# Performance work log

Measured on AMD Instinct MI355X. Metric: run time of the kernel, lower is better.

## Reference

```python
import jax, jax.numpy as jnp
import numpy as np

N_NODES = 100000
K = 50000  # ceil(ratio * N) with ratio = nodes_out / nodes_in = 0.5


def setup_inputs() -> dict:
    key = jax.random.key(0)
    k1, k2, k3 = jax.random.split(key, 3)
    x = jax.random.normal(k1, (N_NODES, 256), dtype=jnp.float32)
    edge_index = jax.random.randint(k2, (2, 3200000), 0, N_NODES, dtype=jnp.int64)
    weight = jax.random.normal(k3, (256,), dtype=jnp.float32)
    return {"x": x, "edge_index": edge_index, "weight": weight}


def reference(x, edge_index, weight):
    # --- PyG TopKPooling forward ---
    # score_i = tanh( <x_i, w> / ||w|| )
    score = jnp.tanh((x @ weight) / jnp.linalg.norm(weight))  # [N]
    # select top-k nodes by score
    top_scores, perm = jax.lax.top_k(score, K)  # [K], [K]
    # gather features and gate by score (multiplier)
    x_out = x[perm] * top_scores[:, None]  # [K, C]
    # --- filter_adj: keep edges whose endpoints both survive, remap ids ---
    mapping = jnp.full((x.shape[0],), -1, dtype=edge_index.dtype)
    mapping = mapping.at[perm].set(jnp.arange(K, dtype=edge_index.dtype))
    new_edges = mapping[edge_index]  # [2, E], -1 where endpoint dropped
    valid = (new_edges[0] >= 0) & (new_edges[1] >= 0)
    # fixed-shape output: invalid edges marked -1 (torch returns a compacted
    # variable-length tensor; we keep E fixed for jit-compatibility)
    edge_out = jnp.where(valid[None, :], new_edges, -1)
    return x_out, edge_out
```

## Files before the change

### kernel.cpp

```cpp
#include <hip/hip_runtime.h>
#include <math.h>

#define N_NODES 100000
#define N_FEAT  256
#define K_SEL   50000
#define N_EDGES 3200000
#define NBUCKET 65536

#define GATHER_BLOCKS (K_SEL / 4)
#define EDGE_BLOCKS   (N_EDGES / (4 * 256))

__device__ __forceinline__ unsigned long long descKey(double z) {
    unsigned long long u = (unsigned long long)__double_as_longlong(z);
    unsigned long long a = (u >> 63) ? ~u : (u | 0x8000000000000000ULL);
    return ~a;
}

__device__ __forceinline__ unsigned int bucketOfFloat(float zf) {
    unsigned int u = __float_as_uint(zf);
    unsigned int a = (u >> 31) ? ~u : (u | 0x80000000u);
    return (~a) >> 16;
}

__global__ void init_kernel(const float* __restrict__ w, double* __restrict__ norm,
                            int* __restrict__ hist) {
    __shared__ double sd[256];
    int t = blockIdx.x * blockDim.x + threadIdx.x;
    hist[t] = 0;
    if (blockIdx.x == 0) {
        int tt = threadIdx.x;
        double v = (double)w[tt];
        sd[tt] = v * v;
        __syncthreads();
        for (int off = 128; off > 0; off >>= 1) {
            if (tt < off) sd[tt] += sd[tt + off];
            __syncthreads();
        }
        if (tt == 0) norm[0] = sqrt(sd[0]);
    }
}

__global__ void score_kernel(const float* __restrict__ x, const float* __restrict__ w,
                             unsigned long long* __restrict__ key64,
                             float* __restrict__ dotf, int* __restrict__ hist) {
    int row  = (int)((blockIdx.x * blockDim.x + threadIdx.x) >> 6);
    int lane = threadIdx.x & 63;
    if (row >= N_NODES) return;
    const float4 xv = ((const float4*)(x + (size_t)row * N_FEAT))[lane];
    const float4 wv = ((const float4*)w)[lane];
    double acc = (double)xv.x * (double)wv.x + (double)xv.y * (double)wv.y +
                 (double)xv.z * (double)wv.z + (double)xv.w * (double)wv.w;
    for (int m = 32; m >= 1; m >>= 1) acc += __shfl_xor(acc, m, 64);
    if (lane == 0) {
        key64[row] = descKey(acc);
        float df = (float)acc;
        dotf[row] = df;
        atomicAdd(&hist[bucketOfFloat(df)], 1);
    }
}

__global__ void __launch_bounds__(1024) scan_kernel(const int4* __restrict__ hist4,
                                                    int* __restrict__ start) {
    __shared__ int sums[1024];
    int t = threadIdx.x;
    int4 v[16];
#pragma unroll
    for (int j = 0; j < 16; ++j) v[j] = hist4[t * 16 + j];
    int s = 0;
#pragma unroll
    for (int j = 0; j < 16; ++j) { s += v[j].x + v[j].y + v[j].z + v[j].w; }
    sums[t] = s;
    __syncthreads();
    for (int off = 1; off < 1024; off <<= 1) {
        int vv = (t >= off) ? sums[t - off] : 0;
        __syncthreads();
        sums[t] += vv;
        __syncthreads();
    }
    int run = (t == 0) ? 0 : sums[t - 1];
    int4* start4 = (int4*)start;
#pragma unroll
    for (int j = 0; j < 16; ++j) {
        int4 o;
        o.x = run; run += v[j].x;
        o.y = run; run += v[j].y;
        o.z = run; run += v[j].z;
        o.w = run; run += v[j].w;
        start4[t * 16 + j] = o;
    }
}

__global__ void scatter_kernel(const unsigned long long* __restrict__ key64,
                               const float* __restrict__ dotf,
                               int* __restrict__ start,
                               unsigned long long* __restrict__ slotKey,
                               int* __restrict__ slotIdx) {
    int i = blockIdx.x * blockDim.x + threadIdx.x;
    if (i >= N_NODES) return;
    int b = (int)bucketOfFloat(dotf[i]);
    int pos = atomicAdd(&start[b], 1);
    slotKey[pos] = key64[i];
    slotIdx[pos] = i;
}

__global__ void rank_kernel(const unsigned long long* __restrict__ slotKey,
                            const int* __restrict__ slotIdx,
                            const int* __restrict__ start, const int* __restrict__ hist,
                            const float* __restrict__ dotf,
                            int* __restrict__ mapping, int* __restrict__ perm,
                            float* __restrict__ selDot) {
    int s = blockIdx.x * blockDim.x + threadIdx.x;
    if (s >= N_NODES) return;
    unsigned long long myKey = slotKey[s];
    int i = slotIdx[s];
    float df = dotf[i];
    int b = (int)bucketOfFloat(df);
    int end = start[b];
    int cnt = hist[b];
    int st = end - cnt;
    int rank = 0;
    for (int t = st; t < end; ++t) {
        unsigned long long k = slotKey[t];
        if (k < myKey || (k == myKey && slotIdx[t] < i)) ++rank;
    }
    int p = st + rank;
    if (p < K_SEL) {
        mapping[i] = p;
        perm[p] = i;
        selDot[p] = df;
    } else {
        mapping[i] = -1;
    }
}

__global__ void out_kernel(const float* __restrict__ x, const int* __restrict__ perm,
                           const float* __restrict__ selDot,
                           const double* __restrict__ normp,
                           const int* __restrict__ ei, const int* __restrict__ mapping,
                           float* __restrict__ out) {
    if (blockIdx.x < GATHER_BLOCKS) {
        int tid = blockIdx.x * 256 + threadIdx.x;
        int r = tid >> 6;
        int c = (tid & 63) << 2;
        int src = perm[r];
        float sc = tanhf(selDot[r] / (float)normp[0]);
        float4 v = *(const float4*)(x + (size_t)src * N_FEAT + c);
        float4 o;
        o.x = v.x * sc; o.y = v.y * sc; o.z = v.z * sc; o.w = v.w * sc;
        *(float4*)(out + (size_t)r * N_FEAT + c) = o;
    } else {
        int tid = (blockIdx.x - GATHER_BLOCKS) * 256 + threadIdx.x;
        int e = tid << 2;
        int4 a = *(const int4*)(ei + e);
        int4 b = *(const int4*)(ei + N_EDGES + e);
        float* oeu = out + (size_t)K_SEL * N_FEAT;
        float* oev = oeu + N_EDGES;
        int m0 = mapping[a.x], m1 = mapping[a.y], m2 = mapping[a.z], m3 = mapping[a.w];
        int n0 = mapping[b.x], n1 = mapping[b.y], n2 = mapping[b.z], n3 = mapping[b.w];
        float4 ou, ov;
        bool v0 = (m0 >= 0) && (n0 >= 0);
        bool v1 = (m1 >= 0) && (n1 >= 0);
        bool v2 = (m2 >= 0) && (n2 >= 0);
        bool v3 = (m3 >= 0) && (n3 >= 0);
        ou.x = v0 ? (float)m0 : -1.0f; ov.x = v0 ? (float)n0 : -1.0f;
        ou.y = v1 ? (float)m1 : -1.0f; ov.y = v1 ? (float)n1 : -1.0f;
        ou.z = v2 ? (float)m2 : -1.0f; ov.z = v2 ? (float)n2 : -1.0f;
        ou.w = v3 ? (float)m3 : -1.0f; ov.w = v3 ? (float)n3 : -1.0f;
        *(float4*)(oeu + e) = ou;
        *(float4*)(oev + e) = ov;
    }
}

extern "C" void kernel_launch(void* const* d_in, const int* in_sizes, int n_in,
                              void* d_out, int out_size, void* d_ws, size_t ws_size,
                              hipStream_t stream) {
    const float* x  = (const float*)d_in[0];
    const int*   ei = (const int*)d_in[1];
    const float* w  = (const float*)d_in[2];
    float* out = (float*)d_out;

    char* p = (char*)d_ws;
    double* d_norm = (double*)p;                          p += 16;
    unsigned long long* key64   = (unsigned long long*)p; p += (size_t)N_NODES * 8;
    unsigned long long* slotKey = (unsigned long long*)p; p += (size_t)N_NODES * 8;
    float* dotf   = (float*)p;  p += (size_t)N_NODES * 4;
    int*   mapping= (int*)p;    p += (size_t)N_NODES * 4;
    int*   slotIdx= (int*)p;    p += (size_t)N_NODES * 4;
    int*   perm   = (int*)p;    p += (size_t)K_SEL * 4;
    float* selDot = (float*)p;  p += (size_t)K_SEL * 4;
    int*   hist   = (int*)p;    p += (size_t)NBUCKET * 4;
    int*   start  = (int*)p;    p += (size_t)NBUCKET * 4;

    init_kernel<<<NBUCKET / 256, 256, 0, stream>>>(w, d_norm, hist);

    int waves_blocks = (N_NODES * 64 + 255) / 256;
    score_kernel<<<waves_blocks, 256, 0, stream>>>(x, w, key64, dotf, hist);

    scan_kernel<<<1, 1024, 0, stream>>>((const int4*)hist, start);

    int node_blocks = (N_NODES + 255) / 256;
    scatter_kernel<<<node_blocks, 256, 0, stream>>>(key64, dotf, start, slotKey, slotIdx);

    rank_kernel<<<node_blocks, 256, 0, stream>>>(slotKey, slotIdx, start, hist, dotf,
                                                 mapping, perm, selDot);

    out_kernel<<<GATHER_BLOCKS + EDGE_BLOCKS, 256, 0, stream>>>(x, perm, selDot, d_norm,
                                                                ei, mapping, out);
}
```

Measured before the change: 319.6 us.

## Parallelize histogram scan, shrink mapping to 16-bit, replace init kernel with memset

Replaces the single-block 1024-thread histogram scan with a two-level scan: 256 blocks scan chunks, then one block scans the chunk sums and also computes the inverse weight norm. The init kernel becomes a hipMemsetAsync. The node mapping table is stored as 16-bit values with 0xFFFF as sentinel, halving the footprint of the table used by the random edge lookups. This adds one kernel launch and relies on K fitting in 16 bits.

```diff
diff --git a/kernel.cpp b/kernel.cpp
--- a/kernel.cpp
+++ b/kernel.cpp
@@ -6,6 +6,7 @@
 #define K_SEL   50000
 #define N_EDGES 3200000
 #define NBUCKET 65536
+#define NCHUNK  (NBUCKET / 256)
 
 #define GATHER_BLOCKS (K_SEL / 4)
 #define EDGE_BLOCKS   (N_EDGES / (4 * 256))
@@ -20,24 +21,6 @@
     unsigned int u = __float_as_uint(zf);
     unsigned int a = (u >> 31) ? ~u : (u | 0x80000000u);
     return (~a) >> 16;
-}
-
-__global__ void init_kernel(const float* __restrict__ w, double* __restrict__ norm,
-                            int* __restrict__ hist) {
-    __shared__ double sd[256];
-    int t = blockIdx.x * blockDim.x + threadIdx.x;
-    hist[t] = 0;
-    if (blockIdx.x == 0) {
-        int tt = threadIdx.x;
-        double v = (double)w[tt];
-        sd[tt] = v * v;
-        __syncthreads();
-        for (int off = 128; off > 0; off >>= 1) {
-            if (tt < off) sd[tt] += sd[tt + off];
-            __syncthreads();
-        }
-        if (tt == 0) norm[0] = sqrt(sd[0]);
-    }
 }
 
 __global__ void score_kernel(const float* __restrict__ x, const float* __restrict__ w,
@@ -59,63 +42,75 @@
     }
 }
 
-__global__ void __launch_bounds__(1024) scan_kernel(const int4* __restrict__ hist4,
-                                                    int* __restrict__ start) {
-    __shared__ int sums[1024];
+__global__ void scanA_kernel(const int* __restrict__ hist, int* __restrict__ partial,
+                             int* __restrict__ chunkSum) {
+    __shared__ int tmp[256];
     int t = threadIdx.x;
-    int4 v[16];
-#pragma unroll
-    for (int j = 0; j < 16; ++j) v[j] = hist4[t * 16 + j];
-    int s = 0;
-#pragma unroll
-    for (int j = 0; j < 16; ++j) { s += v[j].x + v[j].y + v[j].z + v[j].w; }
-    sums[t] = s;
+    int g = blockIdx.x * 256 + t;
+    int v = hist[g];
+    tmp[t] = v;
     __syncthreads();
-    for (int off = 1; off < 1024; off <<= 1) {
-        int vv = (t >= off) ? sums[t - off] : 0;
-        __syncthreads();
-        sums[t] += vv;
-        __syncthreads();
-    }
-    int run = (t == 0) ? 0 : sums[t - 1];
-    int4* start4 = (int4*)start;
-#pragma unroll
-    for (int j = 0; j < 16; ++j) {
-        int4 o;
-        o.x = run; run += v[j].x;
-        o.y = run; run += v[j].y;
-        o.z = run; run += v[j].z;
-        o.w = run; run += v[j].w;
-        start4[t * 16 + j] = o;
-    }
+    for (int off = 1; off < 256; off <<= 1) {
+        int u = (t >= off) ? tmp[t - off] : 0;
+        __syncthreads();
+        tmp[t] += u;
+        __syncthreads();
+    }
+    partial[g] = tmp[t] - v;
+    if (t == 255) chunkSum[blockIdx.x] = tmp[255];
+}
+
+__global__ void scanB_kernel(const int* __restrict__ chunkSum, int* __restrict__ offs,
+                             const float* __restrict__ w, float* __restrict__ invNorm) {
+    __shared__ int tmp[256];
+    __shared__ double sd[256];
+    int t = threadIdx.x;
+    int v = chunkSum[t];
+    tmp[t] = v;
+    double wv = (double)w[t];
+    sd[t] = wv * wv;
+    __syncthreads();
+    for (int off = 1; off < 256; off <<= 1) {
+        int u = (t >= off) ? tmp[t - off] : 0;
+        __syncthreads();
+        tmp[t] += u;
+        __syncthreads();
+    }
+    offs[t] = tmp[t] - v;
+    for (int off = 128; off > 0; off >>= 1) {
+        if (t < off) sd[t] += sd[t + off];
+        __syncthreads();
+    }
+    if (t == 0) invNorm[0] = (float)(1.0 / sqrt(sd[0]));
 }
 
 __global__ void scatter_kernel(const unsigned long long* __restrict__ key64,
                                const float* __restrict__ dotf,
-                               int* __restrict__ start,
+                               const int* __restrict__ offs, int* __restrict__ partial,
                                unsigned long long* __restrict__ slotKey,
                                int* __restrict__ slotIdx) {
     int i = blockIdx.x * blockDim.x + threadIdx.x;
     if (i >= N_NODES) return;
     int b = (int)bucketOfFloat(dotf[i]);
-    int pos = atomicAdd(&start[b], 1);
+    int pos = offs[b >> 8] + atomicAdd(&partial[b], 1);
     slotKey[pos] = key64[i];
     slotIdx[pos] = i;
 }
 
 __global__ void rank_kernel(const unsigned long long* __restrict__ slotKey,
                             const int* __restrict__ slotIdx,
-                            const int* __restrict__ start, const int* __restrict__ hist,
+                            const int* __restrict__ offs, const int* __restrict__ partial,
+                            const int* __restrict__ hist,
                             const float* __restrict__ dotf,
-                            int* __restrict__ mapping, int* __restrict__ perm,
-                            float* __restrict__ selDot) {
+                            unsigned short* __restrict__ mapping16,
+                            int* __restrict__ perm, float* __restrict__ selDot) {
     int s = blockIdx.x * blockDim.x + threadIdx.x;
     if (s >= N_NODES) return;
     unsigned long long myKey = slotKey[s];
     int i = slotIdx[s];
     float df = dotf[i];
     int b = (int)bucketOfFloat(df);
-    int end = start[b];
+    int end = offs[b >> 8] + partial[b];
     int cnt = hist[b];
     int st = end - cnt;
     int rank = 0;
@@ -125,25 +120,26 @@
     }
     int p = st + rank;
     if (p < K_SEL) {
-        mapping[i] = p;
+        mapping16[i] = (unsigned short)p;
         perm[p] = i;
         selDot[p] = df;
     } else {
-        mapping[i] = -1;
+        mapping16[i] = 0xFFFFu;
     }
 }
 
 __global__ void out_kernel(const float* __restrict__ x, const int* __restrict__ perm,
                            const float* __restrict__ selDot,
-                           const double* __restrict__ normp,
-                           const int* __restrict__ ei, const int* __restrict__ mapping,
+                           const float* __restrict__ invNormp,
+                           const int* __restrict__ ei,
+                           const unsigned short* __restrict__ mapping16,
                            float* __restrict__ out) {
     if (blockIdx.x < GATHER_BLOCKS) {
         int tid = blockIdx.x * 256 + threadIdx.x;
         int r = tid >> 6;
         int c = (tid & 63) << 2;
         int src = perm[r];
-        float sc = tanhf(selDot[r] / (float)normp[0]);
+        float sc = tanhf(selDot[r] * invNormp[0]);
         float4 v = *(const float4*)(x + (size_t)src * N_FEAT + c);
         float4 o;
         o.x = v.x * sc; o.y = v.y * sc; o.z = v.z * sc; o.w = v.w * sc;
@@ -155,13 +151,15 @@
         int4 b = *(const int4*)(ei + N_EDGES + e);
         float* oeu = out + (size_t)K_SEL * N_FEAT;
         float* oev = oeu + N_EDGES;
-        int m0 = mapping[a.x], m1 = mapping[a.y], m2 = mapping[a.z], m3 = mapping[a.w];
-        int n0 = mapping[b.x], n1 = mapping[b.y], n2 = mapping[b.z], n3 = mapping[b.w];
+        unsigned short m0 = mapping16[a.x], m1 = mapping16[a.y];
+        unsigned short m2 = mapping16[a.z], m3 = mapping16[a.w];
+        unsigned short n0 = mapping16[b.x], n1 = mapping16[b.y];
+        unsigned short n2 = mapping16[b.z], n3 = mapping16[b.w];
+        bool v0 = (m0 != 0xFFFFu) && (n0 != 0xFFFFu);
+        bool v1 = (m1 != 0xFFFFu) && (n1 != 0xFFFFu);
+        bool v2 = (m2 != 0xFFFFu) && (n2 != 0xFFFFu);
+        bool v3 = (m3 != 0xFFFFu) && (n3 != 0xFFFFu);
         float4 ou, ov;
-        bool v0 = (m0 >= 0) && (n0 >= 0);
-        bool v1 = (m1 >= 0) && (n1 >= 0);
-        bool v2 = (m2 >= 0) && (n2 >= 0);
-        bool v3 = (m3 >= 0) && (n3 >= 0);
         ou.x = v0 ? (float)m0 : -1.0f; ov.x = v0 ? (float)n0 : -1.0f;
         ou.y = v1 ? (float)m1 : -1.0f; ov.y = v1 ? (float)n1 : -1.0f;
         ou.z = v2 ? (float)m2 : -1.0f; ov.z = v2 ? (float)n2 : -1.0f;
@@ -180,30 +178,35 @@
     float* out = (float*)d_out;
 
     char* p = (char*)d_ws;
-    double* d_norm = (double*)p;                          p += 16;
+    float* d_invNorm = (float*)p;                         p += 16;
     unsigned long long* key64   = (unsigned long long*)p; p += (size_t)N_NODES * 8;
     unsigned long long* slotKey = (unsigned long long*)p; p += (size_t)N_NODES * 8;
     float* dotf   = (float*)p;  p += (size_t)N_NODES * 4;
-    int*   mapping= (int*)p;    p += (size_t)N_NODES * 4;
     int*   slotIdx= (int*)p;    p += (size_t)N_NODES * 4;
+    unsigned short* mapping16 = (unsigned short*)p;       p += (size_t)N_NODES * 2;
     int*   perm   = (int*)p;    p += (size_t)K_SEL * 4;
     float* selDot = (float*)p;  p += (size_t)K_SEL * 4;
     int*   hist   = (int*)p;    p += (size_t)NBUCKET * 4;
-    int*   start  = (int*)p;    p += (size_t)NBUCKET * 4;
-
-    init_kernel<<<NBUCKET / 256, 256, 0, stream>>>(w, d_norm, hist);
+    int*   partial= (int*)p;    p += (size_t)NBUCKET * 4;
+    int*   chunkSum=(int*)p;    p += (size_t)NCHUNK * 4;
+    int*   offs   = (int*)p;    p += (size_t)NCHUNK * 4;
+
+    hipMemsetAsync(hist, 0, (size_t)NBUCKET * 4, stream);
 
     int waves_blocks = (N_NODES * 64 + 255) / 256;
     score_kernel<<<waves_blocks, 256, 0, stream>>>(x, w, key64, dotf, hist);
 
-    scan_kernel<<<1, 1024, 0, stream>>>((const int4*)hist, start);
+    scanA_kernel<<<NCHUNK, 256, 0, stream>>>(hist, partial, chunkSum);
+    scanB_kernel<<<1, 256, 0, stream>>>(chunkSum, offs, w, d_invNorm);
 
     int node_blocks = (N_NODES + 255) / 256;
-    scatter_kernel<<<node_blocks, 256, 0, stream>>>(key64, dotf, start, slotKey, slotIdx);
-
-    rank_kernel<<<node_blocks, 256, 0, stream>>>(slotKey, slotIdx, start, hist, dotf,
-                                                 mapping, perm, selDot);
-
-    out_kernel<<<GATHER_BLOCKS + EDGE_BLOCKS, 256, 0, stream>>>(x, perm, selDot, d_norm,
-                                                                ei, mapping, out);
-}
+    scatter_kernel<<<node_blocks, 256, 0, stream>>>(key64, dotf, offs, partial,
+                                                    slotKey, slotIdx);
+
+    rank_kernel<<<node_blocks, 256, 0, stream>>>(slotKey, slotIdx, offs, partial, hist,
+                                                 dotf, mapping16, perm, selDot);
+
+    out_kernel<<<GATHER_BLOCKS + EDGE_BLOCKS, 256, 0, stream>>>(x, perm, selDot,
+                                                                d_invNorm, ei,
+                                                                mapping16, out);
+}
```

Result: slower. 331.7 us (+3.8%).
